# Kernel tuning notes

Measured on AMD Instinct MI355X. Metric: run time of the kernel, lower is better.

Reference implementation:

```python
import jax, jax.numpy as jnp
import numpy as np

B, H, W, C = 8, 64, 64, 512
D = C // 8  # key/query/value projection dim per SAGAN block


def setup_inputs() -> dict:
    key = jax.random.key(0)
    ks = jax.random.split(key, 5)
    scale = 1.0 / np.sqrt(C)
    return {
        "x": jax.random.normal(ks[0], (B, H, W, C), dtype=jnp.float32),
        "Wf": jax.random.normal(ks[1], (C, D), dtype=jnp.float32) * scale,
        "bf": jnp.zeros((D,), dtype=jnp.float32),
        "Wg": jax.random.normal(ks[2], (C, D), dtype=jnp.float32) * scale,
        "bg": jnp.zeros((D,), dtype=jnp.float32),
        "Wh": jax.random.normal(ks[3], (C, D), dtype=jnp.float32) * scale,
        "bh": jnp.zeros((D,), dtype=jnp.float32),
        "Wv": jax.random.normal(ks[4], (D, C), dtype=jnp.float32) * (1.0 / np.sqrt(D)),
        "bv": jnp.zeros((C,), dtype=jnp.float32),
        "gamma": jnp.float32(0.01),
    }


def reference(x, Wf, bf, Wg, bg, Wh, bh, Wv, bv, gamma):
    b, h, w, c = x.shape
    n = h * w
    xf = x.reshape(b, n, c)  # flatten spatial dims: [B, N, C]
    # 1x1 convs == per-position dense projections
    f = xf @ Wf + bf  # [B, N, D]
    g = xf @ Wg + bg  # [B, N, D]
    hh = xf @ Wh + bh  # [B, N, D]
    # unscaled attention logits, softmax over keys (axis=-1)
    s = jnp.einsum("bnd,bmd->bnm", f, g)  # [B, N, N]
    attn = jax.nn.softmax(s, axis=-1)
    context = jnp.einsum("bnm,bmd->bnd", attn, hh)  # [B, N, D]
    # v conv (1x1) applied to gamma-scaled context, residual add
    o = (gamma * context) @ Wv + bv + xf  # [B, N, C]
    return o.reshape(b, h, w, c)
```

## Files before the change

### kernel.cpp

```cpp
#include <hip/hip_runtime.h>
#include <hip/hip_bf16.h>
#include <math.h>


typedef short v8s __attribute__((ext_vector_type(8)));
typedef unsigned short v4u __attribute__((ext_vector_type(4)));
typedef unsigned v4i __attribute__((ext_vector_type(4)));
typedef float v4f __attribute__((ext_vector_type(4)));

#define BB 8
#define NN 4096
#define CC 512
#define DD 64

__device__ __forceinline__ unsigned short f2bf(float f){
  union { float f; unsigned u; } v; v.f = f;
  unsigned r = (v.u + 0x7FFF + ((v.u >> 16) & 1)) >> 16;
  return (unsigned short)r;
}

#if __has_builtin(__builtin_amdgcn_cvt_pk_bf16_f32)
typedef __bf16 bf2_t __attribute__((ext_vector_type(2)));
__device__ __forceinline__ unsigned pkbf(float a, float b){
  bf2_t r = __builtin_amdgcn_cvt_pk_bf16_f32(a, b);
  union { bf2_t v; unsigned u; } c; c.v = r; return c.u;
}
#else
__device__ __forceinline__ unsigned pkbf(float a, float b){
  return (unsigned)f2bf(a) | ((unsigned)f2bf(b) << 16);
}
#endif

#if __has_builtin(__builtin_amdgcn_exp2f)
__device__ __forceinline__ float ex2(float x){ return __builtin_amdgcn_exp2f(x); }
#else
__device__ __forceinline__ float ex2(float x){ return exp2f(x); }
#endif

__device__ __forceinline__ void gload_lds16(const void* g, void* l){
  __builtin_amdgcn_global_load_lds(
      (const __attribute__((address_space(1))) void*)g,
      (__attribute__((address_space(3))) void*)l, 16, 0, 0);
}

__global__ void transpose_w(const float* __restrict__ Wf,
                            const float* __restrict__ Wg,
                            const float* __restrict__ Wh,
                            const float* __restrict__ Wv,
                            unsigned short* __restrict__ Wt,
                            unsigned short* __restrict__ Wvt){
  int idx = blockIdx.x * 256 + threadIdx.x;
  if (idx < 3 * DD * CC){
    int p = idx / (DD * CC); int rem = idx % (DD * CC);
    int d = rem / CC; int c = rem % CC;
    const float* W = (p == 0) ? Wf : ((p == 1) ? Wg : Wh);
    Wt[idx] = f2bf(W[c * DD + d]);
  } else {
    int idx2 = idx - 3 * DD * CC;
    if (idx2 < CC * DD){
      int c = idx2 / DD; int d = idx2 % DD;
      Wvt[idx2] = f2bf(Wv[d * CC + c]);
    }
  }
}

__global__ __launch_bounds__(256) void proj_kernel(
    const float* __restrict__ x,
    const unsigned short* __restrict__ Wt,
    const float* __restrict__ bf_,
    const float* __restrict__ bg_,
    const float* __restrict__ bh_,
    unsigned short* __restrict__ f,
    unsigned short* __restrict__ g,
    unsigned short* __restrict__ ht)
{
  __shared__ __align__(16) short lA[64][72];
  __shared__ __align__(16) short lB[192][72];
  int t = threadIdx.x;
  int w = t >> 6, lane = t & 63;
  int quad = lane >> 4, l16 = lane & 15;
  int rowbase = blockIdx.x * 64;
  int m0 = w * 16;

  v4f acc[12];
  #pragma unroll
  for (int i = 0; i < 12; i++) acc[i] = (v4f){0.f, 0.f, 0.f, 0.f};

  int arow = t >> 2, aq4 = t & 3;
  for (int kt = 0; kt < 8; ++kt){
    int k0 = kt * 64;
    {
      const float* xp = x + (rowbase + arow) * 512 + k0 + aq4 * 16;
      v4f a0 = *(const v4f*)(xp);
      v4f a1 = *(const v4f*)(xp + 4);
      v4f a2 = *(const v4f*)(xp + 8);
      v4f a3 = *(const v4f*)(xp + 12);
      v4i c0 = { pkbf(a0[0],a0[1]), pkbf(a0[2],a0[3]),
                 pkbf(a1[0],a1[1]), pkbf(a1[2],a1[3]) };
      v4i c1 = { pkbf(a2[0],a2[1]), pkbf(a2[2],a2[3]),
                 pkbf(a3[0],a3[1]), pkbf(a3[2],a3[3]) };
      *(v4i*)&lA[arow][aq4 * 16]     = c0;
      *(v4i*)&lA[arow][aq4 * 16 + 8] = c1;
    }
    #pragma unroll
    for (int r = 0; r < 6; r++){
      int chunk = t + r * 256;
      int row = chunk >> 3, c8 = chunk & 7;
      *(v8s*)&lB[row][c8 * 8] = *(const v8s*)(Wt + row * 512 + k0 + c8 * 8);
    }
    __syncthreads();
    v8s A0 = *(const v8s*)&lA[m0 + l16][quad * 8];
    v8s A1 = *(const v8s*)&lA[m0 + l16][quad * 8 + 32];
    #pragma unroll
    for (int cb = 0; cb < 12; ++cb){
      v8s b0 = *(const v8s*)&lB[cb * 16 + l16][quad * 8];
      v8s b1 = *(const v8s*)&lB[cb * 16 + l16][quad * 8 + 32];
      acc[cb] = __builtin_amdgcn_mfma_f32_16x16x32_bf16(A0, b0, acc[cb], 0, 0, 0);
      acc[cb] = __builtin_amdgcn_mfma_f32_16x16x32_bf16(A1, b1, acc[cb], 0, 0, 0);
    }
    __syncthreads();
  }

  #pragma unroll
  for (int cb = 0; cb < 8; ++cb){
    int col = cb * 16 + l16;
    int p = col >> 6, d = col & 63;
    float bb = (p == 0) ? bf_[d] : bg_[d];
    #pragma unroll
    for (int r = 0; r < 4; r++){
      int gr = rowbase + m0 + quad * 4 + r;
      float val = acc[cb][r] + bb;
      if (p == 0) f[gr * 64 + d] = f2bf(val * 1.44269504f);
      else        g[gr * 64 + d] = f2bf(val);
    }
  }

  short (*lT)[65] = (short(*)[65])lB;
  #pragma unroll
  for (int cb = 8; cb < 12; ++cb){
    int d = (cb - 8) * 16 + l16;
    float bb = bh_[d];
    #pragma unroll
    for (int r = 0; r < 4; r++)
      lT[m0 + quad * 4 + r][d] = (short)f2bf(acc[cb][r] + bb);
  }
  __syncthreads();
  {
    int dd = t >> 2, nb = t & 3;
    v8s h0, h1;
    #pragma unroll
    for (int i = 0; i < 8; i++){
      h0[i] = lT[nb * 16 + i][dd];
      h1[i] = lT[nb * 16 + 8 + i][dd];
    }
    int bidx = rowbase >> 12;
    int n0 = (rowbase & 4095) + nb * 16;
    unsigned short* hp = ht + ((size_t)(bidx * 64 + dd)) * 4096 + n0;
    *(v8s*)hp = h0;
    *(v8s*)(hp + 8) = h1;
  }
}

__global__ __launch_bounds__(256) void flash_kernel(
    const unsigned short* __restrict__ f,
    const unsigned short* __restrict__ g,
    const unsigned short* __restrict__ ht,
    float* __restrict__ Opart,
    float* __restrict__ lipart,
    unsigned short* __restrict__ ctx,
    int niter, int direct)
{
  __shared__ __align__(16) short lK[2][64 * 64];
  __shared__ __align__(16) short lV[2][64 * 64];
  __shared__ __align__(16) short lP[4][8][16][8];
  int t = threadIdx.x;
  int w = t >> 6, lane = t & 63;
  int quad = lane >> 4, l16 = lane & 15;
  int qt = blockIdx.x, sp = blockIdx.y, b = blockIdx.z;
  int q0 = qt * 64;
  int m0 = w * 16;

  const unsigned short* fb = f  + b * NN * 64;
  const unsigned short* gb = g  + b * NN * 64;
  const unsigned short* hb = ht + b * 64 * NN;

  v8s QB0 = *(const v8s*)(fb + (q0 + m0 + l16) * 64 + quad * 8);
  v8s QB1 = *(const v8s*)(fb + (q0 + m0 + l16) * 64 + quad * 8 + 32);

  int j0 = sp * niter;
  const char* srcK[2]; const char* srcV[2];
  char* dstK[2][2]; char* dstV[2][2];
  #pragma unroll
  for (int k = 0; k < 2; k++){
    int row = w * 16 + k * 8 + (lane >> 3);
    int c = (lane & 7) ^ (row & 7);
    srcK[k] = (const char*)gb + (size_t)j0 * 8192 + row * 128 + c * 16;
    srcV[k] = (const char*)hb + (size_t)row * 8192 + (size_t)j0 * 128 + c * 16;
    #pragma unroll
    for (int b2 = 0; b2 < 2; b2++){
      dstK[b2][k] = (char*)lK[b2] + w * 2048 + k * 1024;
      dstV[b2][k] = (char*)lV[b2] + w * 2048 + k * 1024;
    }
  }

  int ph = quad ^ (l16 & 7);
  const short* kA0[2]; const short* kA1[2];
  const short* vB0[2]; const short* vB1[2];
  #pragma unroll
  for (int b2 = 0; b2 < 2; b2++){
    kA0[b2] = lK[b2] + l16 * 64 + ph * 8;
    kA1[b2] = lK[b2] + l16 * 64 + (ph ^ 4) * 8;
    vB0[b2] = lV[b2] + l16 * 64 + ph * 8;
    vB1[b2] = lV[b2] + l16 * 64 + (ph ^ 4) * 8;
  }

  v8s ones;
  #pragma unroll
  for (int i = 0; i < 8; i++) ones[i] = (short)0x3F80;

  v4f rz = (v4f){0.f, 0.f, 0.f, 0.f};
  v4f O[4];
  #pragma unroll
  for (int cb = 0; cb < 4; cb++) O[cb] = (v4f){0.f, 0.f, 0.f, 0.f};

  auto stage = [&](int b2){
    #pragma unroll
    for (int k = 0; k < 2; k++){
      gload_lds16(srcK[k], dstK[b2][k]);
      gload_lds16(srcV[k], dstV[b2][k]);
      srcK[k] += 8192; srcV[k] += 128;
    }
  };

  auto compute = [&](int b2){
    v4f st[4];
    __builtin_amdgcn_s_setprio(1);
    #pragma unroll
    for (int cb = 0; cb < 4; cb++){
      v8s a0 = *(const v8s*)(kA0[b2] + cb * 1024);
      v8s a1 = *(const v8s*)(kA1[b2] + cb * 1024);
      v4f z = (v4f){0.f, 0.f, 0.f, 0.f};
      z = __builtin_amdgcn_mfma_f32_16x16x32_bf16(a0, QB0, z, 0, 0, 0);
      st[cb] = __builtin_amdgcn_mfma_f32_16x16x32_bf16(a1, QB1, z, 0, 0, 0);
    }
    __builtin_amdgcn_s_setprio(0);

    #pragma unroll
    for (int cb = 0; cb < 4; cb++){
      float p0 = ex2(st[cb][0]);
      float p1 = ex2(st[cb][1]);
      float p2 = ex2(st[cb][2]);
      float p3 = ex2(st[cb][3]);
      unsigned d0 = __builtin_amdgcn_perm(__float_as_uint(p1), __float_as_uint(p0), 0x07060302u);
      unsigned d1 = __builtin_amdgcn_perm(__float_as_uint(p3), __float_as_uint(p2), 0x07060302u);
      uint2 pk; pk.x = d0; pk.y = d1;
      *(uint2*)&lP[w][cb * 2 + (quad >> 1)][l16][(quad & 1) * 4] = pk;
    }

    v8s PA0 = *(const v8s*)&lP[w][quad][l16][0];
    v8s PA1 = *(const v8s*)&lP[w][quad + 4][l16][0];

    __builtin_amdgcn_s_setprio(1);
    rz = __builtin_amdgcn_mfma_f32_16x16x32_bf16(PA0, ones, rz, 0, 0, 0);
    rz = __builtin_amdgcn_mfma_f32_16x16x32_bf16(PA1, ones, rz, 0, 0, 0);

    #pragma unroll
    for (int cb = 0; cb < 4; cb++){
      v8s vb0 = *(const v8s*)(vB0[b2] + cb * 1024);
      v8s vb1 = *(const v8s*)(vB1[b2] + cb * 1024);
      O[cb] = __builtin_amdgcn_mfma_f32_16x16x32_bf16(PA0, vb0, O[cb], 0, 0, 0);
      O[cb] = __builtin_amdgcn_mfma_f32_16x16x32_bf16(PA1, vb1, O[cb], 0, 0, 0);
    }
    __builtin_amdgcn_s_setprio(0);
  };

  stage(0);
  __syncthreads();
  for (int jj = 0; jj < niter; jj += 2){
    stage(1);
    compute(0);
    __syncthreads();
    if (jj + 2 < niter) stage(0);
    compute(1);
    __syncthreads();
  }

  if (direct){
    float inv[4];
    #pragma unroll
    for (int r = 0; r < 4; r++)
      inv[r] = 1.0f / rz[r];
    #pragma unroll
    for (int cb = 0; cb < 4; cb++)
      #pragma unroll
      for (int r = 0; r < 4; r++){
        int row = q0 + m0 + quad * 4 + r;
        ctx[(b * NN + row) * 64 + cb * 16 + l16] = f2bf(O[cb][r] * inv[r]);
      }
  } else {
    int bf = (b * 64 + qt) * 4 + sp;
    if (l16 == 0){
      #pragma unroll
      for (int r = 0; r < 4; r++)
        lipart[bf * 64 + m0 + quad * 4 + r] = rz[r];
    }
    float* Ob = Opart + (size_t)bf * 4096;
    #pragma unroll
    for (int cb = 0; cb < 4; cb++)
      #pragma unroll
      for (int r = 0; r < 4; r++)
        Ob[(m0 + quad * 4 + r) * 64 + cb * 16 + l16] = O[cb][r];
  }
}

__global__ __launch_bounds__(256) void reduce_kernel(
    const float* __restrict__ Opart,
    const float* __restrict__ lipart,
    unsigned short* __restrict__ ctx)
{
  int i4 = blockIdx.x * 256 + threadIdx.x;
  int bqt = i4 >> 10;
  int rem = (i4 & 1023) << 2;
  int rl  = rem >> 6;
  const float* Ob  = Opart  + (size_t)bqt * 4 * 4096;
  const float* lib = lipart + bqt * 4 * 64;
  v4f s = *(const v4f*)(Ob + rem);
  s = s + *(const v4f*)(Ob + 4096  + rem);
  s = s + *(const v4f*)(Ob + 8192  + rem);
  s = s + *(const v4f*)(Ob + 12288 + rem);
  float li = (lib[rl] + lib[64 + rl]) + (lib[128 + rl] + lib[192 + rl]);
  float inv = 1.0f / li;
  uint2 o; o.x = pkbf(s[0] * inv, s[1] * inv); o.y = pkbf(s[2] * inv, s[3] * inv);
  *(uint2*)(ctx + (size_t)bqt * 4096 + rem) = o;
}

__global__ __launch_bounds__(256) void outproj_kernel(
    const unsigned short* __restrict__ ctx,
    const unsigned short* __restrict__ Wvt,
    const float* __restrict__ bv,
    const float* __restrict__ x,
    const float* __restrict__ gamma_p,
    float* __restrict__ out)
{
  __shared__ __align__(16) short lA[64][72];
  __shared__ __align__(16) short lB[128][72];
  int t = threadIdx.x;
  int w = t >> 6, lane = t & 63;
  int quad = lane >> 4, l16 = lane & 15;
  int rowbase = blockIdx.x * 64;
  int colbase = blockIdx.y * 128;
  float gamma = *gamma_p;

  #pragma unroll
  for (int r = 0; r < 2; r++){
    int chunk = t + r * 256;
    int row = chunk >> 3, c8 = chunk & 7;
    *(v8s*)&lA[row][c8 * 8] = *(const v8s*)(ctx + (rowbase + row) * 64 + c8 * 8);
  }
  #pragma unroll
  for (int r = 0; r < 4; r++){
    int chunk = t + r * 256;
    int row = chunk >> 3, c8 = chunk & 7;
    *(v8s*)&lB[row][c8 * 8] = *(const v8s*)(Wvt + (colbase + row) * 64 + c8 * 8);
  }
  __syncthreads();
  int m0 = w * 16;
  v8s A0 = *(const v8s*)&lA[m0 + l16][quad * 8];
  v8s A1 = *(const v8s*)&lA[m0 + l16][quad * 8 + 32];
  v4f acc[8];
  #pragma unroll
  for (int cb = 0; cb < 8; cb++){
    v8s b0 = *(const v8s*)&lB[cb * 16 + l16][quad * 8];
    v8s b1 = *(const v8s*)&lB[cb * 16 + l16][quad * 8 + 32];
    v4f z = (v4f){0.f, 0.f, 0.f, 0.f};
    z = __builtin_amdgcn_mfma_f32_16x16x32_bf16(A0, b0, z, 0, 0, 0);
    acc[cb] = __builtin_amdgcn_mfma_f32_16x16x32_bf16(A1, b1, z, 0, 0, 0);
  }
  #pragma unroll
  for (int cb = 0; cb < 8; cb++){
    int col = colbase + cb * 16 + l16;
    float bvv = bv[col];
    #pragma unroll
    for (int r = 0; r < 4; r++){
      int gr = rowbase + m0 + quad * 4 + r;
      out[gr * 512 + col] = gamma * acc[cb][r] + bvv + x[gr * 512 + col];
    }
  }
}

extern "C" void kernel_launch(void* const* d_in, const int* in_sizes, int n_in,
                              void* d_out, int out_size, void* d_ws, size_t ws_size,
                              hipStream_t stream) {
  const float* x   = (const float*)d_in[0];
  const float* Wf  = (const float*)d_in[1];
  const float* bf_ = (const float*)d_in[2];
  const float* Wg  = (const float*)d_in[3];
  const float* bg  = (const float*)d_in[4];
  const float* Wh  = (const float*)d_in[5];
  const float* bh  = (const float*)d_in[6];
  const float* Wv  = (const float*)d_in[7];
  const float* bv  = (const float*)d_in[8];
  const float* gam = (const float*)d_in[9];
  float* out = (float*)d_out;

  char* ws = (char*)d_ws;
  unsigned short* Wt  = (unsigned short*)(ws);
  unsigned short* Wvt = (unsigned short*)(ws + 196608);
  unsigned short* f   = (unsigned short*)(ws + 262144);
  unsigned short* g   = (unsigned short*)(ws + 4456448);
  unsigned short* ht  = (unsigned short*)(ws + 8650752);
  unsigned short* ctx = (unsigned short*)(ws + 12845056);
  float* Opart  = (float*)(ws + 17039360);
  float* lipart = (float*)(ws + 50593792);

  transpose_w<<<512, 256, 0, stream>>>(Wf, Wg, Wh, Wv, Wt, Wvt);
  proj_kernel<<<512, 256, 0, stream>>>(x, Wt, bf_, bg, bh, f, g, ht);

  bool split = (ws_size >= (size_t)51118080);
  if (split){
    flash_kernel<<<dim3(64, 4, 8), 256, 0, stream>>>(f, g, ht, Opart, lipart, ctx, 16, 0);
    reduce_kernel<<<2048, 256, 0, stream>>>(Opart, lipart, ctx);
  } else {
    flash_kernel<<<dim3(64, 1, 8), 256, 0, stream>>>(f, g, ht, nullptr, nullptr, ctx, 64, 1);
  }
  outproj_kernel<<<dim3(512, 4), 256, 0, stream>>>(ctx, Wvt, bv, x, gam, out);
}
```

Before: 217.9 us.

## Give each attention wave two 16-row query tiles to reuse K/V fragments

Each flash-attention wave now processes 32 query rows as two 16-row groups, so a block covers 128 queries instead of 64. Every K and V fragment read from LDS feeds twice as many MFMAs, and each block's K/V global loads are spread over twice as many queries. This is meant to cut LDS and global traffic per unit of work. The grid is halved and the partial-result and reduce indexing are updated to match. In exchange, each thread holds more accumulator and score registers, and fewer blocks are launched, which may lower occupancy or latency hiding.

```diff
diff --git a/kernel.cpp b/kernel.cpp
--- a/kernel.cpp
+++ b/kernel.cpp
@@ -172,20 +172,23 @@
 {
   __shared__ __align__(16) short lK[2][64 * 64];
   __shared__ __align__(16) short lV[2][64 * 64];
-  __shared__ __align__(16) short lP[4][8][16][8];
+  __shared__ __align__(16) short lP[4][2][8][16][8];
   int t = threadIdx.x;
   int w = t >> 6, lane = t & 63;
   int quad = lane >> 4, l16 = lane & 15;
   int qt = blockIdx.x, sp = blockIdx.y, b = blockIdx.z;
-  int q0 = qt * 64;
-  int m0 = w * 16;
+  int q0 = qt * 128;
+  int m0 = w * 32;
 
   const unsigned short* fb = f  + b * NN * 64;
   const unsigned short* gb = g  + b * NN * 64;
   const unsigned short* hb = ht + b * 64 * NN;
 
-  v8s QB0 = *(const v8s*)(fb + (q0 + m0 + l16) * 64 + quad * 8);
-  v8s QB1 = *(const v8s*)(fb + (q0 + m0 + l16) * 64 + quad * 8 + 32);
+  const unsigned short* qbase = fb + (q0 + m0 + l16) * 64;
+  v8s QB00 = *(const v8s*)(qbase + quad * 8);
+  v8s QB01 = *(const v8s*)(qbase + quad * 8 + 32);
+  v8s QB10 = *(const v8s*)(qbase + 16 * 64 + quad * 8);
+  v8s QB11 = *(const v8s*)(qbase + 16 * 64 + quad * 8 + 32);
 
   int j0 = sp * niter;
   const char* srcK[2]; const char* srcV[2];
@@ -218,10 +221,14 @@
   #pragma unroll
   for (int i = 0; i < 8; i++) ones[i] = (short)0x3F80;
 
-  v4f rz = (v4f){0.f, 0.f, 0.f, 0.f};
-  v4f O[4];
-  #pragma unroll
-  for (int cb = 0; cb < 4; cb++) O[cb] = (v4f){0.f, 0.f, 0.f, 0.f};
+  v4f rz[2];
+  rz[0] = (v4f){0.f, 0.f, 0.f, 0.f};
+  rz[1] = (v4f){0.f, 0.f, 0.f, 0.f};
+  v4f O[2][4];
+  #pragma unroll
+  for (int gi = 0; gi < 2; gi++)
+    #pragma unroll
+    for (int cb = 0; cb < 4; cb++) O[gi][cb] = (v4f){0.f, 0.f, 0.f, 0.f};
 
   auto stage = [&](int b2){
     #pragma unroll
@@ -233,43 +240,55 @@
   };
 
   auto compute = [&](int b2){
-    v4f st[4];
+    v4f st[2][4];
     __builtin_amdgcn_s_setprio(1);
     #pragma unroll
     for (int cb = 0; cb < 4; cb++){
       v8s a0 = *(const v8s*)(kA0[b2] + cb * 1024);
       v8s a1 = *(const v8s*)(kA1[b2] + cb * 1024);
-      v4f z = (v4f){0.f, 0.f, 0.f, 0.f};
-      z = __builtin_amdgcn_mfma_f32_16x16x32_bf16(a0, QB0, z, 0, 0, 0);
-      st[cb] = __builtin_amdgcn_mfma_f32_16x16x32_bf16(a1, QB1, z, 0, 0, 0);
+      v4f z0 = (v4f){0.f, 0.f, 0.f, 0.f};
+      z0 = __builtin_amdgcn_mfma_f32_16x16x32_bf16(a0, QB00, z0, 0, 0, 0);
+      st[0][cb] = __builtin_amdgcn_mfma_f32_16x16x32_bf16(a1, QB01, z0, 0, 0, 0);
+      v4f z1 = (v4f){0.f, 0.f, 0.f, 0.f};
+      z1 = __builtin_amdgcn_mfma_f32_16x16x32_bf16(a0, QB10, z1, 0, 0, 0);
+      st[1][cb] = __builtin_amdgcn_mfma_f32_16x16x32_bf16(a1, QB11, z1, 0, 0, 0);
     }
     __builtin_amdgcn_s_setprio(0);
 
     #pragma unroll
-    for (int cb = 0; cb < 4; cb++){
-      float p0 = ex2(st[cb][0]);
-      float p1 = ex2(st[cb][1]);
-      float p2 = ex2(st[cb][2]);
-      float p3 = ex2(st[cb][3]);
-      unsigned d0 = __builtin_amdgcn_perm(__float_as_uint(p1), __float_as_uint(p0), 0x07060302u);
-      unsigned d1 = __builtin_amdgcn_perm(__float_as_uint(p3), __float_as_uint(p2), 0x07060302u);
-      uint2 pk; pk.x = d0; pk.y = d1;
-      *(uint2*)&lP[w][cb * 2 + (quad >> 1)][l16][(quad & 1) * 4] = pk;
-    }
-
-    v8s PA0 = *(const v8s*)&lP[w][quad][l16][0];
-    v8s PA1 = *(const v8s*)&lP[w][quad + 4][l16][0];
+    for (int gi = 0; gi < 2; gi++){
+      #pragma unroll
+      for (int cb = 0; cb < 4; cb++){
+        float p0 = ex2(st[gi][cb][0]);
+        float p1 = ex2(st[gi][cb][1]);
+        float p2 = ex2(st[gi][cb][2]);
+        float p3 = ex2(st[gi][cb][3]);
+        unsigned d0 = __builtin_amdgcn_perm(__float_as_uint(p1), __float_as_uint(p0), 0x07060302u);
+        unsigned d1 = __builtin_amdgcn_perm(__float_as_uint(p3), __float_as_uint(p2), 0x07060302u);
+        uint2 pk; pk.x = d0; pk.y = d1;
+        *(uint2*)&lP[w][gi][cb * 2 + (quad >> 1)][l16][(quad & 1) * 4] = pk;
+      }
+    }
+
+    v8s PA00 = *(const v8s*)&lP[w][0][quad][l16][0];
+    v8s PA01 = *(const v8s*)&lP[w][0][quad + 4][l16][0];
+    v8s PA10 = *(const v8s*)&lP[w][1][quad][l16][0];
+    v8s PA11 = *(const v8s*)&lP[w][1][quad + 4][l16][0];
 
     __builtin_amdgcn_s_setprio(1);
-    rz = __builtin_amdgcn_mfma_f32_16x16x32_bf16(PA0, ones, rz, 0, 0, 0);
-    rz = __builtin_amdgcn_mfma_f32_16x16x32_bf16(PA1, ones, rz, 0, 0, 0);
+    rz[0] = __builtin_amdgcn_mfma_f32_16x16x32_bf16(PA00, ones, rz[0], 0, 0, 0);
+    rz[0] = __builtin_amdgcn_mfma_f32_16x16x32_bf16(PA01, ones, rz[0], 0, 0, 0);
+    rz[1] = __builtin_amdgcn_mfma_f32_16x16x32_bf16(PA10, ones, rz[1], 0, 0, 0);
+    rz[1] = __builtin_amdgcn_mfma_f32_16x16x32_bf16(PA11, ones, rz[1], 0, 0, 0);
 
     #pragma unroll
     for (int cb = 0; cb < 4; cb++){
       v8s vb0 = *(const v8s*)(vB0[b2] + cb * 1024);
       v8s vb1 = *(const v8s*)(vB1[b2] + cb * 1024);
-      O[cb] = __builtin_amdgcn_mfma_f32_16x16x32_bf16(PA0, vb0, O[cb], 0, 0, 0);
-      O[cb] = __builtin_amdgcn_mfma_f32_16x16x32_bf16(PA1, vb1, O[cb], 0, 0, 0);
+      O[0][cb] = __builtin_amdgcn_mfma_f32_16x16x32_bf16(PA00, vb0, O[0][cb], 0, 0, 0);
+      O[0][cb] = __builtin_amdgcn_mfma_f32_16x16x32_bf16(PA01, vb1, O[0][cb], 0, 0, 0);
+      O[1][cb] = __builtin_amdgcn_mfma_f32_16x16x32_bf16(PA10, vb0, O[1][cb], 0, 0, 0);
+      O[1][cb] = __builtin_amdgcn_mfma_f32_16x16x32_bf16(PA11, vb1, O[1][cb], 0, 0, 0);
     }
     __builtin_amdgcn_s_setprio(0);
   };
@@ -286,30 +305,37 @@
   }
 
   if (direct){
-    float inv[4];
-    #pragma unroll
-    for (int r = 0; r < 4; r++)
-      inv[r] = 1.0f / rz[r];
-    #pragma unroll
-    for (int cb = 0; cb < 4; cb++)
+    #pragma unroll
+    for (int gi = 0; gi < 2; gi++){
+      float inv[4];
       #pragma unroll
-      for (int r = 0; r < 4; r++){
-        int row = q0 + m0 + quad * 4 + r;
-        ctx[(b * NN + row) * 64 + cb * 16 + l16] = f2bf(O[cb][r] * inv[r]);
-      }
+      for (int r = 0; r < 4; r++)
+        inv[r] = 1.0f / rz[gi][r];
+      #pragma unroll
+      for (int cb = 0; cb < 4; cb++)
+        #pragma unroll
+        for (int r = 0; r < 4; r++){
+          int row = q0 + m0 + gi * 16 + quad * 4 + r;
+          ctx[(b * NN + row) * 64 + cb * 16 + l16] = f2bf(O[gi][cb][r] * inv[r]);
+        }
+    }
   } else {
-    int bf = (b * 64 + qt) * 4 + sp;
+    int bf = (b * 32 + qt) * 4 + sp;
     if (l16 == 0){
       #pragma unroll
-      for (int r = 0; r < 4; r++)
-        lipart[bf * 64 + m0 + quad * 4 + r] = rz[r];
-    }
-    float* Ob = Opart + (size_t)bf * 4096;
-    #pragma unroll
-    for (int cb = 0; cb < 4; cb++)
+      for (int gi = 0; gi < 2; gi++)
+        #pragma unroll
+        for (int r = 0; r < 4; r++)
+          lipart[bf * 128 + m0 + gi * 16 + quad * 4 + r] = rz[gi][r];
+    }
+    float* Ob = Opart + (size_t)bf * 8192;
+    #pragma unroll
+    for (int gi = 0; gi < 2; gi++)
       #pragma unroll
-      for (int r = 0; r < 4; r++)
-        Ob[(m0 + quad * 4 + r) * 64 + cb * 16 + l16] = O[cb][r];
+      for (int cb = 0; cb < 4; cb++)
+        #pragma unroll
+        for (int r = 0; r < 4; r++)
+          Ob[(m0 + gi * 16 + quad * 4 + r) * 64 + cb * 16 + l16] = O[gi][cb][r];
   }
 }
 
@@ -319,19 +345,19 @@
     unsigned short* __restrict__ ctx)
 {
   int i4 = blockIdx.x * 256 + threadIdx.x;
-  int bqt = i4 >> 10;
-  int rem = (i4 & 1023) << 2;
+  int bqt = i4 >> 11;
+  int rem = (i4 & 2047) << 2;
   int rl  = rem >> 6;
-  const float* Ob  = Opart  + (size_t)bqt * 4 * 4096;
-  const float* lib = lipart + bqt * 4 * 64;
+  const float* Ob  = Opart  + (size_t)bqt * 4 * 8192;
+  const float* lib = lipart + bqt * 4 * 128;
   v4f s = *(const v4f*)(Ob + rem);
-  s = s + *(const v4f*)(Ob + 4096  + rem);
   s = s + *(const v4f*)(Ob + 8192  + rem);
-  s = s + *(const v4f*)(Ob + 12288 + rem);
-  float li = (lib[rl] + lib[64 + rl]) + (lib[128 + rl] + lib[192 + rl]);
+  s = s + *(const v4f*)(Ob + 16384 + rem);
+  s = s + *(const v4f*)(Ob + 24576 + rem);
+  float li = (lib[rl] + lib[128 + rl]) + (lib[256 + rl] + lib[384 + rl]);
   float inv = 1.0f / li;
   uint2 o; o.x = pkbf(s[0] * inv, s[1] * inv); o.y = pkbf(s[2] * inv, s[3] * inv);
-  *(uint2*)(ctx + (size_t)bqt * 4096 + rem) = o;
+  *(uint2*)(ctx + (size_t)bqt * 8192 + rem) = o;
 }
 
 __global__ __launch_bounds__(256) void outproj_kernel(
@@ -418,10 +444,10 @@
 
   bool split = (ws_size >= (size_t)51118080);
   if (split){
-    flash_kernel<<<dim3(64, 4, 8), 256, 0, stream>>>(f, g, ht, Opart, lipart, ctx, 16, 0);
+    flash_kernel<<<dim3(32, 4, 8), 256, 0, stream>>>(f, g, ht, Opart, lipart, ctx, 16, 0);
     reduce_kernel<<<2048, 256, 0, stream>>>(Opart, lipart, ctx);
   } else {
-    flash_kernel<<<dim3(64, 1, 8), 256, 0, stream>>>(f, g, ht, nullptr, nullptr, ctx, 64, 1);
+    flash_kernel<<<dim3(32, 1, 8), 256, 0, stream>>>(f, g, ht, nullptr, nullptr, ctx, 64, 1);
   }
   outproj_kernel<<<dim3(512, 4), 256, 0, stream>>>(ctx, Wvt, bv, x, gam, out);
 }
```

New measurement: 213.6 us. 1.02x faster.
